# Performance work log

Measured on AMD Instinct MI355X. Metric: run time of the kernel, lower is better.

## Reference

```python
import jax, jax.numpy as jnp
import numpy as np

EMB = 2048
N_HEADS = 16
HEAD_DIM = EMB // N_HEADS
ROPE_BASE = 10000.0


def _rope_cos_sin(seq_len, head_dim, dtype):
    inv_freq = 1.0 / (ROPE_BASE ** (jnp.arange(0, head_dim, 2, dtype=jnp.float32) / head_dim))
    t = jnp.arange(seq_len, dtype=jnp.float32)
    freqs = jnp.einsum('s,d->sd', t, inv_freq)          # [S, head_dim/2]
    emb = jnp.concatenate([freqs, freqs], axis=-1)       # [S, head_dim]
    return jnp.cos(emb).astype(dtype), jnp.sin(emb).astype(dtype)


def _rotate_half(x):
    x1, x2 = jnp.split(x, 2, axis=-1)
    return jnp.concatenate([-x2, x1], axis=-1)


def _apply_rope(x, cos, sin):
    # x: [B, H, S, D]; cos/sin: [S, D]
    return x * cos[None, None, :, :] + _rotate_half(x) * sin[None, None, :, :]


def setup_inputs() -> dict:
    key = jax.random.key(0)
    k1, k2, k3 = jax.random.split(key, 3)
    B, S = 4, 2048
    x = jax.random.normal(k1, (B, S, EMB), dtype=jnp.float32)
    # Additive causal mask: 0 on/below diagonal, -1e9 above.
    causal = jnp.triu(jnp.full((S, S), -1e9, dtype=jnp.float32), k=1)
    att_mask = causal[None, None, :, :]
    Wqkv = jax.random.normal(k2, (3 * EMB, EMB), dtype=jnp.float32) * (EMB ** -0.5)
    Wout = jax.random.normal(k3, (EMB, EMB), dtype=jnp.float32) * (EMB ** -0.5)
    return {"x": x, "att_mask": att_mask, "Wqkv": Wqkv, "Wout": Wout}


def reference(x, att_mask, Wqkv, Wout):
    B, S, E = x.shape
    qkv = jnp.einsum('bse,fe->bsf', x, Wqkv)             # [B, S, 3E]
    q, k, v = jnp.split(qkv, 3, axis=-1)
    def to_heads(t):
        return t.reshape(B, S, N_HEADS, HEAD_DIM).transpose(0, 2, 1, 3)  # [B,H,S,D]
    q, k, v = to_heads(q), to_heads(k), to_heads(v)
    cos, sin = _rope_cos_sin(S, HEAD_DIM, x.dtype)
    q = _apply_rope(q, cos, sin)
    k = _apply_rope(k, cos, sin)
    scaling = HEAD_DIM ** -0.5
    dots = jnp.einsum('bhqd,bhkd->bhqk', q, k) * scaling
    dots = dots + att_mask
    attn = jax.nn.softmax(dots, axis=-1)
    out = jnp.einsum('bhqk,bhkd->bhqd', attn, v)         # [B,H,S,D]
    out = out.transpose(0, 2, 1, 3).reshape(B, S, E)
    return jnp.einsum('bse,fe->bsf', out, Wout)
```

## Files before the change

### kernel.cpp

```cpp
#include <hip/hip_runtime.h>
#include <stdint.h>

typedef __attribute__((ext_vector_type(8))) short short8_t;
typedef __attribute__((ext_vector_type(4))) float f32x4;

__device__ __forceinline__ short f2bf(float f) {
  union { float f; uint32_t u; } v; v.f = f;
  uint32_t r = v.u + 0x7FFFu + ((v.u >> 16) & 1u);
  return (short)(r >> 16);
}
__device__ __forceinline__ float bf2f(short s) {
  union { uint32_t u; float f; } v; v.u = ((uint32_t)(uint16_t)s) << 16; return v.f;
}
__device__ __forceinline__ void gld16(const void* g, void* l) {
  __builtin_amdgcn_global_load_lds((const __attribute__((address_space(1))) void*)g,
                                   (__attribute__((address_space(3))) void*)l, 16, 0, 0);
}

__global__ __launch_bounds__(256) void conv_kernel(const float* __restrict__ in,
                                                   short* __restrict__ out, int n4) {
  int i = blockIdx.x * 256 + threadIdx.x;
  const int stride = gridDim.x * 256;
  for (; i < n4; i += stride) {
    float4 v = reinterpret_cast<const float4*>(in)[i];
    short4 o;
    o.x = f2bf(v.x); o.y = f2bf(v.y); o.z = f2bf(v.z); o.w = f2bf(v.w);
    reinterpret_cast<short4*>(out)[i] = o;
  }
}

__device__ __forceinline__ void storeC(float* C, size_t i, float v) { C[i] = v; }
__device__ __forceinline__ void storeC(short* C, size_t i, float v) { C[i] = f2bf(v); }

template <typename OT, bool FUSEV>
__global__ __launch_bounds__(512, 2) void gemm8p(const short* __restrict__ A,
                                                 const short* __restrict__ B,
                                                 OT* __restrict__ C,
                                                 short* __restrict__ VT,
                                                 int M, int N, int K) {
  __shared__ __align__(16) short lds[65536];
  const int tid = threadIdx.x, lane = tid & 63, w = tid >> 6;
  const int wr = w >> 2, wc = w & 3;
  const int c = lane & 15, g4 = lane >> 4;
  const int xcd = (int)blockIdx.x & 7;
  const int t = (int)blockIdx.x >> 3;
  const int bx = (t & 7) + 8 * (t >> 5);
  const int by = xcd * 4 + ((t >> 3) & 3);
  const size_t m0 = (size_t)by * 256, n0 = (size_t)bx * 256;
  const size_t Kb = (size_t)K * 2;
  const char* Ab = (const char*)A + m0 * Kb;
  const char* Bb = (const char*)B + n0 * Kb;
  const char* aq[2];
  const char* bq[2];
#pragma unroll
  for (int i = 0; i < 2; ++i) {
    const size_t ro = (size_t)((i * 8 + w) * 16 + c) * Kb + g4 * 16;
    aq[i] = Ab + ro;
    bq[i] = Bb + ro;
  }
  char* alds = (char*)lds;
  const int aoff = wr * 8192 + lane * 16;
  const int boff = 65536 + wc * 4096 + lane * 16;
  f32x4 acc[8][4] = {};
  const int NT = K >> 6, NIT = NT >> 1;

  short8_t af[2][4], bfr[2][4];

#define STAGE(q, srcoff, ldsbase)                                  \
  gld16((q)[0] + (srcoff), alds + (ldsbase) + (w << 10));          \
  gld16((q)[1] + (srcoff), alds + (ldsbase) + ((8 + w) << 10))

  STAGE(aq, 0, 0);
  STAGE(bq, 0, 65536);
  STAGE(aq, 64, 16384);
  STAGE(bq, 64, 81920);
  STAGE(aq, 128, 32768);
  STAGE(bq, 128, 98304);
  asm volatile("s_waitcnt vmcnt(0)" ::: "memory");
  asm volatile("s_barrier" ::: "memory");

#define RD_A(S, mi, OFF) \
  asm volatile("ds_read_b128 %0, %1 offset:%c2" : "=v"(af[S][mi]) : "v"(aoff), "i"(OFF))
#define RD_B(S, ni, OFF) \
  asm volatile("ds_read_b128 %0, %1 offset:%c2" : "=v"(bfr[S][ni]) : "v"(boff), "i"(OFF))

#define PREF_A(S, BSEL, KS, MQ)                           \
  RD_A(S, 0, (BSEL) + (KS)*16384 + ((MQ)*4 + 0) * 1024);  \
  RD_A(S, 1, (BSEL) + (KS)*16384 + ((MQ)*4 + 1) * 1024);  \
  RD_A(S, 2, (BSEL) + (KS)*16384 + ((MQ)*4 + 2) * 1024);  \
  RD_A(S, 3, (BSEL) + (KS)*16384 + ((MQ)*4 + 3) * 1024)

#define PREF_B(S, BSEL, KS)                  \
  RD_B(S, 0, (BSEL) + (KS)*16384 + 0);       \
  RD_B(S, 1, (BSEL) + (KS)*16384 + 1024);    \
  RD_B(S, 2, (BSEL) + (KS)*16384 + 2048);    \
  RD_B(S, 3, (BSEL) + (KS)*16384 + 3072)

#define MFMA16(AS, BS, MQ)                                                               \
  __builtin_amdgcn_s_setprio(1);                                                         \
  _Pragma("unroll") for (int mi = 0; mi < 4; ++mi) {                                     \
    _Pragma("unroll") for (int n = 0; n < 4; ++n)                                        \
      acc[(MQ)*4 + mi][n] = __builtin_amdgcn_mfma_f32_16x16x32_bf16(                     \
          af[AS][mi], bfr[BS][n], acc[(MQ)*4 + mi][n], 0, 0, 0);                         \
  }                                                                                      \
  __builtin_amdgcn_s_setprio(0)

#define PHASE_E(AS, BS, PBSEL, PKS, q, srcoff, sbase)              \
  PREF_A(AS ^ 1, PBSEL, PKS, 1);                                   \
  STAGE(q, srcoff, sbase);                                         \
  asm volatile("s_waitcnt lgkmcnt(4)" ::: "memory");               \
  __builtin_amdgcn_sched_barrier(0);                               \
  MFMA16(AS, BS, 0);                                               \
  asm volatile("s_barrier" ::: "memory")

#define PHASE_O(AS, BS, PBSEL, PKS, q, srcoff, sbase, GATE)        \
  PREF_B(BS ^ 1, PBSEL, PKS);                                      \
  PREF_A(AS ^ 1, PBSEL, PKS, 0);                                   \
  STAGE(q, srcoff, sbase);                                         \
  asm volatile("s_waitcnt lgkmcnt(8)" ::: "memory");               \
  __builtin_amdgcn_sched_barrier(0);                               \
  MFMA16(AS, BS, 1);                                               \
  GATE;                                                            \
  asm volatile("s_barrier" ::: "memory")

#define GATE8 asm volatile("s_waitcnt vmcnt(8)" ::: "memory")
#define GATE4 asm volatile("s_waitcnt vmcnt(4)" ::: "memory")
#define NOGATE (void)0

  PREF_B(0, 0, 0);
  PREF_A(0, 0, 0, 0);

  for (int it = 0; it < NIT; ++it) {
    const int T = it << 1;
    const int t1 = (T + 1) << 7;
    const int t2 = (T + 2 < NT ? T + 2 : NT - 1) << 7;
    const int t3 = (T + 3 < NT ? T + 3 : NT - 1) << 7;
    PHASE_E(0, 0, 0, 0,      aq, t1 + 64, 49152);
    PHASE_O(1, 0, 0, 1,      bq, t1 + 64, 114688, NOGATE);
    PHASE_E(0, 1, 0, 1,      aq, t2, 0);
    PHASE_O(1, 1, 32768, 0,  bq, t2, 65536, GATE8);
    PHASE_E(0, 0, 32768, 0,  aq, t2 + 64, 16384);
    PHASE_O(1, 0, 32768, 1,  bq, t2 + 64, 81920, NOGATE);
    PHASE_E(0, 1, 32768, 1,  aq, t3, 32768);
    PHASE_O(1, 1, 0, 0,      bq, t3, 98304, GATE4);
  }
#undef PHASE_E
#undef PHASE_O
#undef GATE8
#undef GATE4
#undef NOGATE
#undef MFMA16
#undef PREF_A
#undef PREF_B
#undef RD_A
#undef RD_B
#undef STAGE

#pragma unroll
  for (int m = 0; m < 8; ++m)
#pragma unroll
    for (int n = 0; n < 4; ++n) {
      const size_t col = n0 + wc * 64 + n * 16 + c;
      const size_t rb = m0 + wr * 128 + m * 16 + g4 * 4;
      bool tovt = false;
      if constexpr (FUSEV) tovt = (col >= 4096);
      if (tovt) {
        const size_t cc = col - 4096;
        const size_t b = rb >> 11, s0 = rb & 2047;
        short4 o;
        o.x = f2bf(acc[m][n][0]); o.y = f2bf(acc[m][n][1]);
        o.z = f2bf(acc[m][n][2]); o.w = f2bf(acc[m][n][3]);
        *(short4*)&VT[(b * 2048 + cc) * 2048 + s0] = o;
      } else {
#pragma unroll
        for (int r = 0; r < 4; ++r) storeC(C, (rb + r) * (size_t)N + col, acc[m][n][r]);
      }
    }
}

__global__ __launch_bounds__(256) void rope_kernel(short* __restrict__ qkv) {
  const int g = blockIdx.x * 256 + threadIdx.x;
  const int jg = g & 7;
  const int h = (g >> 3) & 15;
  const int bs = g >> 7;
  const int s = bs & 2047;
  const size_t base = (size_t)bs * 6144 + 2048 + h * 128 + jg * 8;
  short8_t lo = *(short8_t*)&qkv[base];
  short8_t hi = *(short8_t*)&qkv[base + 64];
  short8_t olo, ohi;
#pragma unroll
  for (int t = 0; t < 8; ++t) {
    const int j = jg * 8 + t;
    const float inv = exp2f((float)j * -0.20762050593046f);
    float sn, cn;
    sincosf((float)s * inv, &sn, &cn);
    const float a = bf2f(lo[t]), b = bf2f(hi[t]);
    olo[t] = f2bf(a * cn - b * sn);
    ohi[t] = f2bf(b * cn + a * sn);
  }
  *(short8_t*)&qkv[base] = olo;
  *(short8_t*)&qkv[base + 64] = ohi;
}

__global__ __launch_bounds__(256) void attn_kernel(const short* __restrict__ qkv,
                                                   const short* __restrict__ vt,
                                                   short* __restrict__ o) {
  __shared__ __align__(16) short Kl[2][64 * 128];
  __shared__ __align__(16) short Vl[2][128 * 64];
  __shared__ __align__(16) short Pl[4][16 * 72];
  const int tid = threadIdx.x, lane = tid & 63, w = tid >> 6;
  const int c = lane & 15, g4 = lane >> 4;
  const int blk = blockIdx.x;
  const int xcd = blk & 7;
  const int l = blk >> 3;
  const int bh = xcd * 8 + (l >> 5);
  const int h = bh & 15, b = bh >> 4;
  const int q0 = (31 - (l & 31)) * 64;
  const int srow = q0 + w * 16 + c;

  short8_t qf[4];
  {
    const size_t qr = ((size_t)b * 2048 + srow) * 6144 + h * 128;
    float fl[4][8];
#pragma unroll
    for (int dc = 0; dc < 4; ++dc) {
      short8_t rawv = *(const short8_t*)&qkv[qr + dc * 32 + g4 * 8];
#pragma unroll
      for (int t = 0; t < 8; ++t) fl[dc][t] = bf2f(rawv[t]);
    }
#pragma unroll
    for (int pd = 0; pd < 2; ++pd)
#pragma unroll
      for (int t = 0; t < 8; ++t) {
        const int j = pd * 32 + g4 * 8 + t;
        const float inv = exp2f((float)j * -0.20762050593046f);
        float sn, cn;
        sincosf((float)srow * inv, &sn, &cn);
        const float a = fl[pd][t], bb = fl[pd + 2][t];
        fl[pd][t] = a * cn - bb * sn;
        fl[pd + 2][t] = bb * cn + a * sn;
      }
#pragma unroll
    for (int dc = 0; dc < 4; ++dc) {
      short8_t q8;
#pragma unroll
      for (int t = 0; t < 8; ++t) q8[t] = f2bf(fl[dc][t]);
      qf[dc] = q8;
    }
  }

  f32x4 acc_o[8] = {};
  float rs[4] = {0.f, 0.f, 0.f, 0.f};
  const float scale2 = 0.12751875222364685f;
  const char* Kbase = (const char*)qkv + ((size_t)b * 2048 * 6144 + 2048 + h * 128) * 2;
  const char* Vbase = (const char*)vt + ((size_t)(b * 16 + h) * 128 * 2048) * 2;

  const char* kq[4];
  const char* vq[4];
#pragma unroll
  for (int i = 0; i < 4; ++i) {
    const int L = ((w * 4 + i) << 10) + lane * 16;
    {
      const int row = L >> 8, inner = L & 255;
      kq[i] = Kbase + (size_t)row * 12288 + (inner ^ ((row & 7) << 4));
    }
    {
      const int row = L >> 7, inner = L & 127;
      vq[i] = Vbase + (size_t)row * 4096 + (inner ^ ((row & 7) << 4));
    }
  }
  auto stage = [&](int buf, int kv0) {
#pragma unroll
    for (int i = 0; i < 4; ++i) {
      gld16(kq[i] + (size_t)kv0 * 12288, (char*)Kl + (buf << 14) + ((w * 4 + i) << 10));
      gld16(vq[i] + (size_t)kv0 * 2, (char*)Vl + (buf << 14) + ((w * 4 + i) << 10));
    }
  };

  stage(0, 0);
  __syncthreads();
  int cur = 0;
  for (int kv0 = 0; kv0 <= q0; kv0 += 64) {
    if (kv0 + 64 <= q0) stage(cur ^ 1, kv0 + 64);
    const char* Kb = (const char*)Kl + (cur << 14);
    const char* Vb = (const char*)Vl + (cur << 14);
    const bool diag = (kv0 == q0);
    float p[4][4];
#pragma unroll
    for (int kt = 0; kt < 4; ++kt) {
      f32x4 s4 = {};
      const int krow = kt * 16 + c;
      __builtin_amdgcn_s_setprio(1);
#pragma unroll
      for (int dc = 0; dc < 4; ++dc) {
        const int inner = (dc * 64 + g4 * 16) ^ ((krow & 7) << 4);
        short8_t kf = *(const short8_t*)(Kb + krow * 256 + inner);
        s4 = __builtin_amdgcn_mfma_f32_16x16x32_bf16(qf[dc], kf, s4, 0, 0, 0);
      }
      __builtin_amdgcn_s_setprio(0);
#pragma unroll
      for (int r = 0; r < 4; ++r) {
        float v = s4[r] * scale2 - 8.0f;
        if (diag) {
          const int kc = kv0 + kt * 16 + c;
          const int qr2 = q0 + w * 16 + g4 * 4 + r;
          if (kc > qr2) v = -1e30f;
        }
        const float pe = exp2f(v);
        p[kt][r] = pe;
        rs[r] += pe;
      }
    }
#pragma unroll
    for (int kt = 0; kt < 4; ++kt)
#pragma unroll
      for (int r = 0; r < 4; r += 2) {
        uint32_t pk;
        asm("v_cvt_pk_bf16_f32 %0, %1, %2" : "=v"(pk) : "v"(p[kt][r]), "v"(p[kt][r + 1]));
        Pl[w][(g4 * 4 + r) * 72 + kt * 16 + c] = (short)(pk & 0xffffu);
        Pl[w][(g4 * 4 + r + 1) * 72 + kt * 16 + c] = (short)(pk >> 16);
      }
#pragma unroll
    for (int kk = 0; kk < 2; ++kk) {
      short8_t pf = *(const short8_t*)&Pl[w][c * 72 + kk * 32 + g4 * 8];
      __builtin_amdgcn_s_setprio(1);
#pragma unroll
      for (int dt = 0; dt < 8; ++dt) {
        const int vrow = dt * 16 + c;
        const int inner = (kk * 64 + g4 * 16) ^ ((vrow & 7) << 4);
        short8_t vf = *(const short8_t*)(Vb + vrow * 128 + inner);
        acc_o[dt] = __builtin_amdgcn_mfma_f32_16x16x32_bf16(pf, vf, acc_o[dt], 0, 0, 0);
      }
      __builtin_amdgcn_s_setprio(0);
    }
    __syncthreads();
    cur ^= 1;
  }
#pragma unroll
  for (int off = 1; off < 16; off <<= 1)
#pragma unroll
    for (int r = 0; r < 4; ++r) rs[r] += __shfl_xor(rs[r], off);
  const size_t ob = ((size_t)b * 2048 + q0 + w * 16 + g4 * 4) * 2048 + h * 128;
#pragma unroll
  for (int dt = 0; dt < 8; ++dt)
#pragma unroll
    for (int r = 0; r < 4; ++r)
      o[ob + (size_t)r * 2048 + dt * 16 + c] = f2bf(acc_o[dt][r] / rs[r]);
}

extern "C" void kernel_launch(void* const* d_in, const int* in_sizes, int n_in,
                              void* d_out, int out_size, void* d_ws, size_t ws_size,
                              hipStream_t stream) {
  const float* x = (const float*)d_in[0];
  const float* Wqkv = (const float*)d_in[2];
  const float* Wout = (const float*)d_in[3];
  float* out = (float*)d_out;
  char* ws = (char*)d_ws;
  short* xb   = (short*)ws;
  short* wqb  = (short*)(ws + 33554432ull);
  short* qkv  = (short*)(ws + 58720256ull);
  short* vt   = (short*)(ws + 159383552ull);
  short* attno = xb;
  short* woutb = wqb;

  conv_kernel<<<2048, 256, 0, stream>>>(x, xb, 16777216 / 4);
  conv_kernel<<<2048, 256, 0, stream>>>(Wqkv, wqb, 12582912 / 4);
  gemm8p<short, true><<<768, 512, 0, stream>>>(xb, wqb, qkv, vt, 8192, 6144, 2048);
  conv_kernel<<<2048, 256, 0, stream>>>(Wout, woutb, 4194304 / 4);
  rope_kernel<<<4096, 256, 0, stream>>>(qkv);
  attn_kernel<<<2048, 256, 0, stream>>>(qkv, vt, attno);
  gemm8p<float, false><<<256, 512, 0, stream>>>(attno, woutb, out, nullptr, 8192, 2048, 2048);
}
```

Measured before the change: 517.8 us.

## Merge fp32-to-bf16 conversions into one launch and halve attention KV tile

Replaces the three separate conversion launches with one kernel that converts x, Wqkv and Wout in a single grid-stride pass. Wout's bf16 copy now goes to a separate workspace region instead of reusing the Wqkv buffer. The attention kernel's KV tile shrinks from 64 to 32 rows, halving K/V/P shared memory per block to raise occupancy and reduce wasted causal work on the diagonal. The cost is twice as many loop iterations and barriers, and half as many MFMAs per step between syncs.

```diff
diff --git a/kernel.cpp b/kernel.cpp
--- a/kernel.cpp
+++ b/kernel.cpp
@@ -17,15 +17,25 @@
                                    (__attribute__((address_space(3))) void*)l, 16, 0, 0);
 }
 
-__global__ __launch_bounds__(256) void conv_kernel(const float* __restrict__ in,
-                                                   short* __restrict__ out, int n4) {
+__global__ __launch_bounds__(256) void conv3_kernel(const float* __restrict__ x,
+                                                    const float* __restrict__ wqkv,
+                                                    const float* __restrict__ wout,
+                                                    short* __restrict__ xb,
+                                                    short* __restrict__ wqb,
+                                                    short* __restrict__ woutb) {
   int i = blockIdx.x * 256 + threadIdx.x;
   const int stride = gridDim.x * 256;
-  for (; i < n4; i += stride) {
-    float4 v = reinterpret_cast<const float4*>(in)[i];
+  for (; i < 8388608; i += stride) {
+    const float4* src;
+    short4* dst;
+    int j;
+    if (i < 4194304) { src = (const float4*)x; dst = (short4*)xb; j = i; }
+    else if (i < 7340032) { src = (const float4*)wqkv; dst = (short4*)wqb; j = i - 4194304; }
+    else { src = (const float4*)wout; dst = (short4*)woutb; j = i - 7340032; }
+    float4 v = src[j];
     short4 o;
     o.x = f2bf(v.x); o.y = f2bf(v.y); o.z = f2bf(v.z); o.w = f2bf(v.w);
-    reinterpret_cast<short4*>(out)[i] = o;
+    dst[j] = o;
   }
 }
 
@@ -205,9 +215,9 @@
 __global__ __launch_bounds__(256) void attn_kernel(const short* __restrict__ qkv,
                                                    const short* __restrict__ vt,
                                                    short* __restrict__ o) {
-  __shared__ __align__(16) short Kl[2][64 * 128];
-  __shared__ __align__(16) short Vl[2][128 * 64];
-  __shared__ __align__(16) short Pl[4][16 * 72];
+  __shared__ __align__(16) short Kl[2][32 * 128];
+  __shared__ __align__(16) short Vl[2][128 * 32];
+  __shared__ __align__(16) short Pl[4][16 * 40];
   const int tid = threadIdx.x, lane = tid & 63, w = tid >> 6;
   const int c = lane & 15, g4 = lane >> 4;
   const int blk = blockIdx.x;
@@ -255,39 +265,40 @@
   const char* Kbase = (const char*)qkv + ((size_t)b * 2048 * 6144 + 2048 + h * 128) * 2;
   const char* Vbase = (const char*)vt + ((size_t)(b * 16 + h) * 128 * 2048) * 2;
 
-  const char* kq[4];
-  const char* vq[4];
-#pragma unroll
-  for (int i = 0; i < 4; ++i) {
-    const int L = ((w * 4 + i) << 10) + lane * 16;
+  const char* kq[2];
+  const char* vq[2];
+#pragma unroll
+  for (int i = 0; i < 2; ++i) {
+    const int L = ((w * 2 + i) << 10) + lane * 16;
     {
       const int row = L >> 8, inner = L & 255;
       kq[i] = Kbase + (size_t)row * 12288 + (inner ^ ((row & 7) << 4));
     }
     {
-      const int row = L >> 7, inner = L & 127;
-      vq[i] = Vbase + (size_t)row * 4096 + (inner ^ ((row & 7) << 4));
+      const int row = L >> 6, inner = L & 63;
+      vq[i] = Vbase + (size_t)row * 4096 + (inner ^ ((row & 3) << 4));
     }
   }
   auto stage = [&](int buf, int kv0) {
 #pragma unroll
-    for (int i = 0; i < 4; ++i) {
-      gld16(kq[i] + (size_t)kv0 * 12288, (char*)Kl + (buf << 14) + ((w * 4 + i) << 10));
-      gld16(vq[i] + (size_t)kv0 * 2, (char*)Vl + (buf << 14) + ((w * 4 + i) << 10));
+    for (int i = 0; i < 2; ++i) {
+      gld16(kq[i] + (size_t)kv0 * 12288, (char*)Kl + (buf << 13) + ((w * 2 + i) << 10));
+      gld16(vq[i] + (size_t)kv0 * 2, (char*)Vl + (buf << 13) + ((w * 2 + i) << 10));
     }
   };
 
   stage(0, 0);
   __syncthreads();
   int cur = 0;
-  for (int kv0 = 0; kv0 <= q0; kv0 += 64) {
-    if (kv0 + 64 <= q0) stage(cur ^ 1, kv0 + 64);
-    const char* Kb = (const char*)Kl + (cur << 14);
-    const char* Vb = (const char*)Vl + (cur << 14);
-    const bool diag = (kv0 == q0);
-    float p[4][4];
-#pragma unroll
-    for (int kt = 0; kt < 4; ++kt) {
+  const int kvend = q0 + 32;
+  for (int kv0 = 0; kv0 <= kvend; kv0 += 32) {
+    if (kv0 <= q0) stage(cur ^ 1, kv0 + 32);
+    const char* Kb = (const char*)Kl + (cur << 13);
+    const char* Vb = (const char*)Vl + (cur << 13);
+    const bool diag = (kv0 >= q0);
+    float p[2][4];
+#pragma unroll
+    for (int kt = 0; kt < 2; ++kt) {
       f32x4 s4 = {};
       const int krow = kt * 16 + c;
       __builtin_amdgcn_s_setprio(1);
@@ -312,23 +323,22 @@
       }
     }
 #pragma unroll
-    for (int kt = 0; kt < 4; ++kt)
+    for (int kt = 0; kt < 2; ++kt)
 #pragma unroll
       for (int r = 0; r < 4; r += 2) {
         uint32_t pk;
         asm("v_cvt_pk_bf16_f32 %0, %1, %2" : "=v"(pk) : "v"(p[kt][r]), "v"(p[kt][r + 1]));
-        Pl[w][(g4 * 4 + r) * 72 + kt * 16 + c] = (short)(pk & 0xffffu);
-        Pl[w][(g4 * 4 + r + 1) * 72 + kt * 16 + c] = (short)(pk >> 16);
-      }
-#pragma unroll
-    for (int kk = 0; kk < 2; ++kk) {
-      short8_t pf = *(const short8_t*)&Pl[w][c * 72 + kk * 32 + g4 * 8];
+        Pl[w][(g4 * 4 + r) * 40 + kt * 16 + c] = (short)(pk & 0xffffu);
+        Pl[w][(g4 * 4 + r + 1) * 40 + kt * 16 + c] = (short)(pk >> 16);
+      }
+    {
+      short8_t pf = *(const short8_t*)&Pl[w][c * 40 + g4 * 8];
       __builtin_amdgcn_s_setprio(1);
 #pragma unroll
       for (int dt = 0; dt < 8; ++dt) {
         const int vrow = dt * 16 + c;
-        const int inner = (kk * 64 + g4 * 16) ^ ((vrow & 7) << 4);
-        short8_t vf = *(const short8_t*)(Vb + vrow * 128 + inner);
+        const int inner = (g4 * 16) ^ ((vrow & 3) << 4);
+        short8_t vf = *(const short8_t*)(Vb + vrow * 64 + inner);
         acc_o[dt] = __builtin_amdgcn_mfma_f32_16x16x32_bf16(pf, vf, acc_o[dt], 0, 0, 0);
       }
       __builtin_amdgcn_s_setprio(0);
@@ -361,12 +371,11 @@
   short* qkv  = (short*)(ws + 58720256ull);
   short* vt   = (short*)(ws + 159383552ull);
   short* attno = xb;
-  short* woutb = wqb;
-
-  conv_kernel<<<2048, 256, 0, stream>>>(x, xb, 16777216 / 4);
-  conv_kernel<<<2048, 256, 0, stream>>>(Wqkv, wqb, 12582912 / 4);
+  short* woutb = wqb + 6291456;
+  woutb = (short*)(ws + 192937984ull);
+
+  conv3_kernel<<<2048, 256, 0, stream>>>(x, Wqkv, Wout, xb, wqb, woutb);
   gemm8p<short, true><<<768, 512, 0, stream>>>(xb, wqb, qkv, vt, 8192, 6144, 2048);
-  conv_kernel<<<2048, 256, 0, stream>>>(Wout, woutb, 4194304 / 4);
   rope_kernel<<<4096, 256, 0, stream>>>(qkv);
   attn_kernel<<<2048, 256, 0, stream>>>(qkv, vt, attno);
   gemm8p<float, false><<<256, 512, 0, stream>>>(attno, woutb, out, nullptr, 8192, 2048, 2048);
```

New measurement: 503.9 us. 2.7% less time.
